# Kernel tuning notes

Hardware: AMD Instinct MI355X
Metric: run time of the kernel (lower is better)

## Reference

```python
import jax, jax.numpy as jnp
import numpy as np

B, S, E, H = 512, 128, 256, 256   # batch, seq_len, dim_embedding, dim_model (must be equal per source)
N_GLIMPSE = 1
SAMPLE_SEED = 1


def setup_inputs() -> dict:
    key = jax.random.key(0)
    ks = jax.random.split(key, 24)
    def u(k, shape, scale):
        return jax.random.uniform(k, shape, jnp.float32, -scale, scale)
    s = 1.0 / np.sqrt(H)
    return {
        "problems": jax.random.normal(ks[0], (B, S, 4), jnp.float32),
        # GraphEmbedding: linear 4 -> E
        "embed_W": u(ks[1], (4, E), 0.5),
        "embed_b": u(ks[2], (E,), 0.5),
        # encoder LSTM (PyTorch gate order i,f,g,o; b = b_ih + b_hh)
        "Wi_enc": u(ks[3], (4 * H, E), s),
        "Wh_enc": u(ks[4], (4 * H, H), s),
        "b_enc": u(ks[5], (4 * H,), s),
        # decoder LSTM
        "Wi_dec": u(ks[6], (4 * H, E), s),
        "Wh_dec": u(ks[7], (4 * H, H), s),
        "b_dec": u(ks[8], (4 * H,), s),
        # learned first decoder input
        "dec0": u(ks[9], (H,), s),
        # glimpse Bahdanau attention
        "Wq_g": u(ks[10], (H, H), s), "bq_g": u(ks[11], (H,), s),
        "Wr_g": u(ks[12], (H, H), s), "br_g": u(ks[13], (H,), s),
        "V_g": u(ks[14], (H,), s),
        # pointer Bahdanau attention
        "Wq_p": u(ks[15], (H, H), s), "bq_p": u(ks[16], (H,), s),
        "Wr_p": u(ks[17], (H, H), s), "br_p": u(ks[18], (H,), s),
        "V_p": u(ks[19], (H,), s),
    }


def _lstm_cell(x, h, c, Wi, Wh, b):
    g = x @ Wi.T + h @ Wh.T + b
    i, f, gg, o = jnp.split(g, 4, axis=-1)
    c = jax.nn.sigmoid(f) * c + jax.nn.sigmoid(i) * jnp.tanh(gg)
    h = jax.nn.sigmoid(o) * jnp.tanh(c)
    return h, c


def reference(problems, embed_W, embed_b, Wi_enc, Wh_enc, b_enc, Wi_dec, Wh_dec, b_dec,
              dec0, Wq_g, bq_g, Wr_g, br_g, V_g, Wq_p, bq_p, Wr_p, br_p, V_p):
    nb, sl = problems.shape[0], problems.shape[1]
    embd = problems @ embed_W + embed_b  # [B,S,E]

    h0 = jnp.zeros((nb, H), jnp.float32)
    def enc_step(carry, x):
        h, c = carry
        h, c = _lstm_cell(x, h, c, Wi_enc, Wh_enc, b_enc)
        return (h, c), h
    (h, c), hs = jax.lax.scan(enc_step, (h0, h0), embd.transpose(1, 0, 2))
    enc = hs.transpose(1, 0, 2)  # [B,S,H] encoder states

    # L_ref is a 1x1 conv == per-position linear; it only depends on enc, hoist out of loop
    refp_g = enc @ Wr_g.T + br_g  # [B,S,H]
    refp_p = enc @ Wr_p.T + br_p

    def attn(q, refp, Wq, bq, V):
        qp = q @ Wq.T + bq  # [B,H]
        # U[b,s] = sum_d V[d] * tanh(qp[b,d] + refp[b,s,d]) * 10
        return jnp.einsum('bsd,d->bs', jnp.tanh(qp[:, None, :] + refp) * 10.0, V)

    key = jax.random.key(SAMPLE_SEED)
    bidx = jnp.arange(nb)

    def dec_step(carry, _):
        h, c, last, visited, t = carry
        x = jnp.where(t == 0, dec0[None, :], embd[bidx, last])  # [B,E]
        h, c = _lstm_cell(x, h, c, Wi_dec, Wh_dec, b_dec)
        q = h
        for _g in range(N_GLIMPSE):
            u = attn(q, refp_g, Wq_g, bq_g, V_g)
            u = jnp.where(visited, -1e8, u)  # mask already-chosen actions
            q = jnp.einsum('bsd,bs->bd', refp_g, jax.nn.softmax(u, axis=1))
        logits = attn(q, refp_p, Wq_p, bq_p, V_p)
        logits = jnp.where(visited, -jnp.inf, logits)
        act = jax.random.categorical(jax.random.fold_in(key, t), logits)  # 'sampling'
        probs = jax.nn.softmax(logits, axis=1)
        p_sel = jnp.take_along_axis(probs, act[:, None], axis=1)[:, 0]
        visited = visited.at[bidx, act].set(True)
        return (h, c, act, visited, t + 1), (p_sel, act)

    carry0 = (h, c, jnp.zeros((nb,), jnp.int32), jnp.zeros((nb, sl), bool), jnp.int32(0))
    _, (probs_seq, acts) = jax.lax.scan(dec_step, carry0, None, length=sl)
    return probs_seq, acts  # [S,B] float probs of chosen actions, [S,B] int actions
```

## Files before the change

### kernel.cpp

```cpp
#include <hip/hip_runtime.h>
#include <math.h>
#include <stdint.h>

#define NB 512
#define SL 128

#define O_WHEF    0
#define O_WHDF    262144
#define O_WRT     524288
#define O_WQGT    655360
#define O_WQPT    720896
#define O_ME64    786432
#define O_MD64    794624
#define O_VE64    802816
#define O_VD64    804864
#define O_X064    806912
#define O_HDH     808960
#define O_HDC     1071104
#define O_RG      1333248
#define O_RP      18110464
#define O_HALL    34887680
#define O_GUM     51664896
#define WS_FLOATS 68442112

__device__ __align__(16) float g_ws[WS_FLOATS];

__device__ __forceinline__ float sigf(float x) { return 1.0f / (1.0f + expf(-x)); }

__device__ __forceinline__ float tanh_fast(float x) {
    float e = __expf(2.0f * x);
    return 1.0f - 2.0f / (e + 1.0f);
}

__device__ __forceinline__ void tf2x32(uint32_t k0, uint32_t k1, uint32_t x0, uint32_t x1,
                                       uint32_t& o0, uint32_t& o1) {
    uint32_t ks2 = k0 ^ k1 ^ 0x1BD11BDAu;
    x0 += k0; x1 += k1;
#define RR(r) { x0 += x1; x1 = (x1 << r) | (x1 >> (32 - r)); x1 ^= x0; }
    RR(13) RR(15) RR(26) RR(6)   x0 += k1;  x1 += ks2 + 1u;
    RR(17) RR(29) RR(16) RR(24)  x0 += ks2; x1 += k0 + 2u;
    RR(13) RR(15) RR(26) RR(6)   x0 += k0;  x1 += k1 + 3u;
    RR(17) RR(29) RR(16) RR(24)  x0 += k1;  x1 += ks2 + 4u;
    RR(13) RR(15) RR(26) RR(6)   x0 += ks2; x1 += k0 + 5u;
#undef RR
    o0 = x0; o1 = x1;
}

__device__ __forceinline__ double gumbel_jax(uint32_t k0, uint32_t k1, uint32_t n) {
    uint32_t o0, o1; tf2x32(k0, k1, 0u, n, o0, o1);
    uint32_t bits = o0 ^ o1;
    float f = __uint_as_float((bits >> 9) | 0x3f800000u) - 1.0f;
    f = fmaxf(f, 1.17549435e-38f);
    return -log(-log((double)f));
}

__global__ void pre_k(const float* __restrict__ embed_W, const float* __restrict__ embed_b,
                      const float* __restrict__ Wi_enc, const float* __restrict__ Wh_enc,
                      const float* __restrict__ b_enc,
                      const float* __restrict__ Wi_dec, const float* __restrict__ Wh_dec,
                      const float* __restrict__ b_dec, const float* __restrict__ dec0,
                      const float* __restrict__ Wr_g, const float* __restrict__ Wr_p,
                      const float* __restrict__ Wq_g, const float* __restrict__ Wq_p) {
    float* ws = g_ws;
    double* ME = (double*)(ws + O_ME64);
    double* MD = (double*)(ws + O_MD64);
    double* VE = (double*)(ws + O_VE64);
    double* VD = (double*)(ws + O_VD64);
    double* X0 = (double*)(ws + O_X064);
    double* GUM = (double*)(ws + O_GUM);
    int i0 = blockIdx.x * blockDim.x + threadIdx.x;
    int np = gridDim.x * blockDim.x;
    for (int i = i0; i < 262144; i += np) {
        int k = i >> 10, r = i & 1023;
        int dst = ((k >> 2) << 12) + (r << 2) + (k & 3);
        ws[O_WHEF + dst] = Wh_enc[r * 256 + k];
        ws[O_WHDF + dst] = Wh_dec[r * 256 + k];
    }
    for (int i = i0; i < 131072; i += np) {
        int k = i >> 9, col = i & 511;
        ws[O_WRT + i] = (col < 256) ? Wr_g[col * 256 + k] : Wr_p[(col - 256) * 256 + k];
    }
    for (int i = i0; i < 65536; i += np) {
        int j = i & 255, k = i >> 8;
        int dst = ((k >> 2) << 10) + (j << 2) + (k & 3);
        ws[O_WQGT + dst] = Wq_g[j * 256 + k];
        ws[O_WQPT + dst] = Wq_p[j * 256 + k];
    }
    for (int i = i0; i < 4096; i += np) {
        int e = i >> 10, r = i & 1023;
        const float* we = embed_W + e * 256;
        const float* wa = Wi_enc + r * 256;
        const float* wb = Wi_dec + r * 256;
        double a = 0.0, b = 0.0;
        for (int E = 0; E < 256; ++E) { a += (double)we[E] * wa[E]; b += (double)we[E] * wb[E]; }
        ME[i] = a; MD[i] = b;
    }
    for (int r = i0; r < 1024; r += np) {
        const float* wa = Wi_enc + r * 256;
        const float* wb = Wi_dec + r * 256;
        double a = 0.0, b = 0.0, x = 0.0;
        for (int E = 0; E < 256; ++E) {
            a += (double)embed_b[E] * wa[E];
            b += (double)embed_b[E] * wb[E];
            x += (double)dec0[E] * wb[E];
        }
        VE[r] = a + (double)b_enc[r];
        VD[r] = b + (double)b_dec[r];
        X0[r] = x + (double)b_dec[r];
    }
    for (int i = i0; i < 8388608; i += np) {
        int t = i >> 16;
        uint32_t n = (uint32_t)(i & 65535);
        uint32_t kk0, kk1;
        tf2x32(0u, 1u, 0u, (uint32_t)t, kk0, kk1);
        GUM[i] = gumbel_jax(kk0, kk1, n);
    }
}

__global__ __launch_bounds__(1024) void enc_k(const float* __restrict__ problems) {
    float* ws = g_ws;
    const float4* Wh4 = (const float4*)(ws + O_WHEF);
    const double* ME = (const double*)(ws + O_ME64);
    const double* VE = (const double*)(ws + O_VE64);
    double* HDH = (double*)(ws + O_HDH);
    double* HDC = (double*)(ws + O_HDC);
    float* Hall = ws + O_HALL;

    const int bid = blockIdx.x, tid = threadIdx.x;
    const int b0 = bid << 1;
    __shared__ __align__(16) float hf[2][256];
    __shared__ double gbuf[2][4][256];
    const float4* hf40 = (const float4*)hf[0];
    const float4* hf41 = (const float4*)hf[1];

    if (tid < 512) hf[tid >> 8][tid & 255] = 0.f;
    double c = 0.0;
    __syncthreads();

    const int g = tid >> 8, j = tid & 255;
    const double vE = VE[tid];
    const double m0 = ME[tid], m1 = ME[1024 + tid], m2 = ME[2048 + tid], m3 = ME[3072 + tid];

    for (int t = 0; t < SL; ++t) {
        float4 p0 = *(const float4*)(problems + ((size_t)b0 * SL + t) * 4);
        float4 p1 = *(const float4*)(problems + ((size_t)(b0 + 1) * SL + t) * 4);
        double a0 = vE + (double)p0.x * m0 + (double)p0.y * m1 + (double)p0.z * m2 + (double)p0.w * m3;
        double a1 = vE + (double)p1.x * m0 + (double)p1.y * m1 + (double)p1.z * m2 + (double)p1.w * m3;
        if (t > 0) {
            float f0 = 0.f, f1 = 0.f;
#pragma unroll 4
            for (int k4 = 0; k4 < 64; ++k4) {
                float4 w = Wh4[(k4 << 10) + tid];
                float4 h0 = hf40[k4], h1 = hf41[k4];
                f0 = fmaf(h0.x, w.x, f0); f1 = fmaf(h1.x, w.x, f1);
                f0 = fmaf(h0.y, w.y, f0); f1 = fmaf(h1.y, w.y, f1);
                f0 = fmaf(h0.z, w.z, f0); f1 = fmaf(h1.z, w.z, f1);
                f0 = fmaf(h0.w, w.w, f0); f1 = fmaf(h1.w, w.w, f1);
            }
            a0 += (double)f0;
            a1 += (double)f1;
        }
        gbuf[0][g][j] = a0;
        gbuf[1][g][j] = a1;
        __syncthreads();
        if (tid < 512) {
            int bb = tid >> 8, jj = tid & 255;
            double g0 = gbuf[bb][0][jj], g1 = gbuf[bb][1][jj];
            double g2 = gbuf[bb][2][jj], g3 = gbuf[bb][3][jj];
            float ig = sigf((float)g0), fg = sigf((float)g1), gt = tanhf((float)g2), og = sigf((float)g3);
            c = (double)fg * c + (double)ig * (double)gt;
            double h = (double)og * (double)tanhf((float)c);
            hf[bb][jj] = (float)h;
            Hall[((size_t)(b0 + bb) * SL + t) * 256 + jj] = (float)h;
            if (t == SL - 1) {
                HDH[(size_t)(b0 + bb) * 256 + jj] = h;
                HDC[(size_t)(b0 + bb) * 256 + jj] = c;
            }
        }
        __syncthreads();
    }
}

__global__ __launch_bounds__(256) void refp_gemm(const float* __restrict__ br_g,
                                                 const float* __restrict__ br_p) {
    float* ws = g_ws;
    const float* H = ws + O_HALL;
    const float* W = ws + O_WRT;
    const int bm = blockIdx.x, bn = blockIdx.y;
    const int tid = threadIdx.x;
    const int tr = tid >> 4, tc = tid & 15;
    __shared__ float As[32][65];
    __shared__ float Bs[32][65];
    float acc[4][4] = {};
    for (int kt = 0; kt < 8; ++kt) {
#pragma unroll
        for (int it = 0; it < 8; ++it) {
            int idx = it * 256 + tid;
            int m = idx >> 5, kk = idx & 31;
            As[kk][m] = H[(size_t)(bm * 64 + m) * 256 + kt * 32 + kk];
        }
#pragma unroll
        for (int it = 0; it < 8; ++it) {
            int idx = it * 256 + tid;
            int bk = idx >> 6, bc = idx & 63;
            Bs[bk][bc] = W[(size_t)(kt * 32 + bk) * 512 + bn * 64 + bc];
        }
        __syncthreads();
#pragma unroll
        for (int kk = 0; kk < 32; ++kk) {
            float a0 = As[kk][tr*4+0], a1 = As[kk][tr*4+1], a2 = As[kk][tr*4+2], a3 = As[kk][tr*4+3];
            float b0 = Bs[kk][tc*4+0], b1 = Bs[kk][tc*4+1], b2 = Bs[kk][tc*4+2], b3 = Bs[kk][tc*4+3];
            acc[0][0] = fmaf(a0,b0,acc[0][0]); acc[0][1] = fmaf(a0,b1,acc[0][1]);
            acc[0][2] = fmaf(a0,b2,acc[0][2]); acc[0][3] = fmaf(a0,b3,acc[0][3]);
            acc[1][0] = fmaf(a1,b0,acc[1][0]); acc[1][1] = fmaf(a1,b1,acc[1][1]);
            acc[1][2] = fmaf(a1,b2,acc[1][2]); acc[1][3] = fmaf(a1,b3,acc[1][3]);
            acc[2][0] = fmaf(a2,b0,acc[2][0]); acc[2][1] = fmaf(a2,b1,acc[2][1]);
            acc[2][2] = fmaf(a2,b2,acc[2][2]); acc[2][3] = fmaf(a2,b3,acc[2][3]);
            acc[3][0] = fmaf(a3,b0,acc[3][0]); acc[3][1] = fmaf(a3,b1,acc[3][1]);
            acc[3][2] = fmaf(a3,b2,acc[3][2]); acc[3][3] = fmaf(a3,b3,acc[3][3]);
        }
        __syncthreads();
    }
    const int colg = bn * 64 + tc * 4;
    float4 bias;
    float* outb;
    int colo;
    if (bn < 4) { bias = *(const float4*)(br_g + colg); outb = ws + O_RG; colo = colg; }
    else        { bias = *(const float4*)(br_p + colg - 256); outb = ws + O_RP; colo = colg - 256; }
#pragma unroll
    for (int i = 0; i < 4; ++i) {
        int row = bm * 64 + tr * 4 + i;
        float4 v = make_float4(acc[i][0] + bias.x, acc[i][1] + bias.y,
                               acc[i][2] + bias.z, acc[i][3] + bias.w);
        *(float4*)(outb + (size_t)row * 256 + colo) = v;
    }
}

__global__ __launch_bounds__(1024) void dec_k(const float* __restrict__ problems,
                                              const float* __restrict__ bq_g, const float* __restrict__ Vg,
                                              const float* __restrict__ bq_p, const float* __restrict__ Vp,
                                              float* __restrict__ out) {
    float* ws = g_ws;
    const float4* Wh4 = (const float4*)(ws + O_WHDF);
    const float4* WQG4 = (const float4*)(ws + O_WQGT);
    const float4* WQP4 = (const float4*)(ws + O_WQPT);
    const double* MD = (const double*)(ws + O_MD64);
    const double* VD = (const double*)(ws + O_VD64);
    const double* X0 = (const double*)(ws + O_X064);
    const double* HDH = (const double*)(ws + O_HDH);
    const double* HDC = (const double*)(ws + O_HDC);
    const double* GUM = (const double*)(ws + O_GUM);

    const int b = blockIdx.x, tid = threadIdx.x;
    __shared__ float refg_l[128][256];
    __shared__ __align__(16) float hf[256];
    __shared__ __align__(16) char scr[8192];
    double (*gbuf)[256] = (double(*)[256])scr;
    float  (*pA)[256]   = (float(*)[256])scr;
    float  (*pQ)[256]   = (float(*)[256])(scr + 4096);
    __shared__ __align__(16) float pP[4][256];
    __shared__ float u_l[128];
    __shared__ float w_l[128];
    __shared__ unsigned char vis[128];
    __shared__ int lastA;
    const float4* hf4 = (const float4*)hf;

    {
        const float4* src = (const float4*)(ws + O_RG + (size_t)b * SL * 256);
        float4* dst = (float4*)&refg_l[0][0];
        for (int i = tid; i < 8192; i += 1024) dst[i] = src[i];
    }
    double c = 0.0;
    if (tid < 256) {
        hf[tid] = (float)HDH[(size_t)b * 256 + tid];
        c = HDC[(size_t)b * 256 + tid];
    }
    if (tid < 128) vis[tid] = 0;
    if (tid == 0) lastA = 0;
    __syncthreads();

    const int g = tid >> 8, j = tid & 255;
    const int kq = tid >> 8, jj = tid & 255;
    const int wave = tid >> 6, lane = tid & 63;
    const int d0 = lane, d1 = lane + 64, d2 = lane + 128, d3 = lane + 192;
    const double vD = VD[tid], x0v = X0[tid];
    const double md0 = MD[tid], md1 = MD[1024 + tid], md2 = MD[2048 + tid], md3 = MD[3072 + tid];
    const float* refp = ws + O_RP + (size_t)b * SL * 256;
    const float* prb = problems + (size_t)b * SL * 4;

    for (int t = 0; t < SL; ++t) {
        double a0;
        if (t == 0) {
            a0 = x0v;
        } else {
            float4 p = *(const float4*)(prb + (lastA << 2));
            a0 = vD + (double)p.x * md0 + (double)p.y * md1 + (double)p.z * md2 + (double)p.w * md3;
        }
        {
            float f0 = 0.f;
#pragma unroll 4
            for (int k4 = 0; k4 < 64; ++k4) {
                float4 w = Wh4[(k4 << 10) + tid];
                float4 h = hf4[k4];
                f0 = fmaf(h.x, w.x, f0);
                f0 = fmaf(h.y, w.y, f0);
                f0 = fmaf(h.z, w.z, f0);
                f0 = fmaf(h.w, w.w, f0);
            }
            a0 += (double)f0;
        }
        gbuf[g][j] = a0;
        __syncthreads();
        if (tid < 256) {
            double g0 = gbuf[0][tid], g1 = gbuf[1][tid], g2 = gbuf[2][tid], g3 = gbuf[3][tid];
            float ig = sigf((float)g0), fg = sigf((float)g1), gt = tanhf((float)g2), og = sigf((float)g3);
            c = (double)fg * c + (double)ig * (double)gt;
            double h = (double)og * (double)tanhf((float)c);
            hf[tid] = (float)h;
        }
        __syncthreads();

        {
            const int kb4 = kq << 4;
            float qa = 0.f;
#pragma unroll 4
            for (int kk4 = 0; kk4 < 16; ++kk4) {
                float4 wq = WQG4[((kb4 + kk4) << 8) + jj];
                float4 h = hf4[kb4 + kk4];
                qa = fmaf(h.x, wq.x, qa);
                qa = fmaf(h.y, wq.y, qa);
                qa = fmaf(h.z, wq.z, qa);
                qa = fmaf(h.w, wq.w, qa);
            }
            pA[kq][jj] = qa;
        }
        __syncthreads();
        {
            const float q0 = pA[0][d0] + pA[1][d0] + pA[2][d0] + pA[3][d0] + bq_g[d0], v0 = Vg[d0];
            const float q1 = pA[0][d1] + pA[1][d1] + pA[2][d1] + pA[3][d1] + bq_g[d1], v1 = Vg[d1];
            const float q2 = pA[0][d2] + pA[1][d2] + pA[2][d2] + pA[3][d2] + bq_g[d2], v2 = Vg[d2];
            const float q3 = pA[0][d3] + pA[1][d3] + pA[2][d3] + pA[3][d3] + bq_g[d3], v3 = Vg[d3];
            const int s0 = wave << 3;
            for (int s = s0; s < s0 + 8; ++s) {
                if (vis[s]) continue;
                const float* r0 = refg_l[s];
                float part = tanh_fast(q0 + r0[d0]) * 10.f * v0;
                part = fmaf(tanh_fast(q1 + r0[d1]) * 10.f, v1, part);
                part = fmaf(tanh_fast(q2 + r0[d2]) * 10.f, v2, part);
                part = fmaf(tanh_fast(q3 + r0[d3]) * 10.f, v3, part);
                for (int off = 32; off; off >>= 1) part += __shfl_xor(part, off, 64);
                if (lane == 0) u_l[s] = part;
            }
        }
        __syncthreads();
        if (wave == 0) {
            int s1 = lane, s2 = lane + 64;
            bool v1 = vis[s1], v2 = vis[s2];
            float m = fmaxf(v1 ? -1e30f : u_l[s1], v2 ? -1e30f : u_l[s2]);
            for (int off = 32; off; off >>= 1) m = fmaxf(m, __shfl_xor(m, off, 64));
            float e1 = v1 ? 0.f : expf(u_l[s1] - m);
            float e2 = v2 ? 0.f : expf(u_l[s2] - m);
            float den = e1 + e2;
            for (int off = 32; off; off >>= 1) den += __shfl_xor(den, off, 64);
            w_l[s1] = e1 / den;
            w_l[s2] = e2 / den;
        }
        __syncthreads();
        {
            const int s0 = kq << 5;
            float q = 0.f;
            for (int s = s0; s < s0 + 32; ++s) {
                float w = w_l[s];
                if (w != 0.f) q = fmaf(w, refg_l[s][jj], q);
            }
            pQ[kq][jj] = q;
        }
        __syncthreads();
        {
            const int kb4 = kq << 4;
            float qa = 0.f;
            const float4* pQ0 = (const float4*)pQ[0];
            const float4* pQ1 = (const float4*)pQ[1];
            const float4* pQ2 = (const float4*)pQ[2];
            const float4* pQ3 = (const float4*)pQ[3];
#pragma unroll 4
            for (int kk4 = 0; kk4 < 16; ++kk4) {
                int k4 = kb4 + kk4;
                float4 wq = WQP4[(k4 << 8) + jj];
                float4 q0v = pQ0[k4], q1v = pQ1[k4], q2v = pQ2[k4], q3v = pQ3[k4];
                float qkx = ((q0v.x + q1v.x) + q2v.x) + q3v.x;
                float qky = ((q0v.y + q1v.y) + q2v.y) + q3v.y;
                float qkz = ((q0v.z + q1v.z) + q2v.z) + q3v.z;
                float qkw = ((q0v.w + q1v.w) + q2v.w) + q3v.w;
                qa = fmaf(qkx, wq.x, qa);
                qa = fmaf(qky, wq.y, qa);
                qa = fmaf(qkz, wq.z, qa);
                qa = fmaf(qkw, wq.w, qa);
            }
            pP[kq][jj] = qa;
        }
        __syncthreads();
        {
            const float q0 = pP[0][d0] + pP[1][d0] + pP[2][d0] + pP[3][d0] + bq_p[d0], v0 = Vp[d0];
            const float q1 = pP[0][d1] + pP[1][d1] + pP[2][d1] + pP[3][d1] + bq_p[d1], v1 = Vp[d1];
            const float q2 = pP[0][d2] + pP[1][d2] + pP[2][d2] + pP[3][d2] + bq_p[d2], v2 = Vp[d2];
            const float q3 = pP[0][d3] + pP[1][d3] + pP[2][d3] + pP[3][d3] + bq_p[d3], v3 = Vp[d3];
            const int s0 = wave << 3;
            for (int s = s0; s < s0 + 8; ++s) {
                if (vis[s]) continue;
                const float* r0 = refp + (s << 8);
                float part = tanh_fast(q0 + r0[d0]) * 10.f * v0;
                part = fmaf(tanh_fast(q1 + r0[d1]) * 10.f, v1, part);
                part = fmaf(tanh_fast(q2 + r0[d2]) * 10.f, v2, part);
                part = fmaf(tanh_fast(q3 + r0[d3]) * 10.f, v3, part);
                for (int off = 32; off; off >>= 1) part += __shfl_xor(part, off, 64);
                if (lane == 0) u_l[s] = part;
            }
        }
        __syncthreads();
        if (wave == 0) {
            int s1 = lane, s2 = lane + 64;
            bool v1 = vis[s1], v2 = vis[s2];
            float m = fmaxf(v1 ? -1e30f : u_l[s1], v2 ? -1e30f : u_l[s2]);
            for (int off = 32; off; off >>= 1) m = fmaxf(m, __shfl_xor(m, off, 64));
            float e1 = v1 ? 0.f : expf(u_l[s1] - m);
            float e2 = v2 ? 0.f : expf(u_l[s2] - m);
            float den = e1 + e2;
            for (int off = 32; off; off >>= 1) den += __shfl_xor(den, off, 64);
            const double* gt = GUM + ((size_t)t << 16) + (b << 7);
            double z1 = v1 ? -1.0e300 : (double)u_l[s1] + gt[s1];
            double z2 = v2 ? -1.0e300 : (double)u_l[s2] + gt[s2];
            double bz; int bi;
            if (z2 > z1) { bz = z2; bi = s2; } else { bz = z1; bi = s1; }
            for (int off = 32; off; off >>= 1) {
                double oz = __shfl_xor(bz, off, 64);
                int oi = __shfl_xor(bi, off, 64);
                if (oz > bz || (oz == bz && oi < bi)) { bz = oz; bi = oi; }
            }
            if (lane == 0) {
                float pr = expf(u_l[bi] - m) / den;
                out[t * NB + b] = pr;
                out[SL * NB + t * NB + b] = (float)bi;
                vis[bi] = 1;
                lastA = bi;
            }
        }
        __syncthreads();
    }
}

extern "C" void kernel_launch(void* const* d_in, const int* in_sizes, int n_in,
                              void* d_out, int out_size, void* d_ws, size_t ws_size,
                              hipStream_t stream) {
    (void)d_ws; (void)ws_size; (void)n_in; (void)in_sizes; (void)out_size;
    const float* problems = (const float*)d_in[0];
    const float* embed_W  = (const float*)d_in[1];
    const float* embed_b  = (const float*)d_in[2];
    const float* Wi_enc   = (const float*)d_in[3];
    const float* Wh_enc   = (const float*)d_in[4];
    const float* b_enc    = (const float*)d_in[5];
    const float* Wi_dec   = (const float*)d_in[6];
    const float* Wh_dec   = (const float*)d_in[7];
    const float* b_dec    = (const float*)d_in[8];
    const float* dec0     = (const float*)d_in[9];
    const float* Wq_g     = (const float*)d_in[10];
    const float* bq_g     = (const float*)d_in[11];
    const float* Wr_g     = (const float*)d_in[12];
    const float* br_g     = (const float*)d_in[13];
    const float* V_g      = (const float*)d_in[14];
    const float* Wq_p     = (const float*)d_in[15];
    const float* bq_p     = (const float*)d_in[16];
    const float* Wr_p     = (const float*)d_in[17];
    const float* br_p     = (const float*)d_in[18];
    const float* V_p      = (const float*)d_in[19];
    float* outp = (float*)d_out;

    hipLaunchKernelGGL(pre_k, dim3(512), dim3(256), 0, stream,
                       embed_W, embed_b, Wi_enc, Wh_enc, b_enc,
                       Wi_dec, Wh_dec, b_dec, dec0, Wr_g, Wr_p, Wq_g, Wq_p);
    hipLaunchKernelGGL(enc_k, dim3(256), dim3(1024), 0, stream, problems);
    hipLaunchKernelGGL(refp_gemm, dim3(1024, 8), dim3(256), 0, stream, br_g, br_p);
    hipLaunchKernelGGL(dec_k, dim3(512), dim3(1024), 0, stream,
                       problems, bq_g, V_g, bq_p, V_p, outp);
}
```

Measured before the change: 9.000 ms.

## Overlap next-step LSTM recurrent matvec with attention via split thread groups

```diff
diff --git a/kernel.cpp b/kernel.cpp
--- a/kernel.cpp
+++ b/kernel.cpp
@@ -254,11 +254,12 @@
     const int b = blockIdx.x, tid = threadIdx.x;
     __shared__ float refg_l[128][256];
     __shared__ __align__(16) float hf[256];
+    __shared__ float gpre[1024];
     __shared__ __align__(16) char scr[8192];
     double (*gbuf)[256] = (double(*)[256])scr;
     float  (*pA)[256]   = (float(*)[256])scr;
-    float  (*pQ)[256]   = (float(*)[256])(scr + 4096);
-    __shared__ __align__(16) float pP[4][256];
+    float  (*pQ)[256]   = (float(*)[256])(scr + 2048);
+    float  (*pP)[256]   = (float(*)[256])(scr + 4096);
     __shared__ float u_l[128];
     __shared__ float w_l[128];
     __shared__ unsigned char vis[128];
@@ -279,14 +280,47 @@
     if (tid == 0) lastA = 0;
     __syncthreads();
 
+    {
+        float f0 = 0.f;
+#pragma unroll 4
+        for (int k4 = 0; k4 < 64; ++k4) {
+            float4 w = Wh4[(k4 << 10) + tid];
+            float4 h = hf4[k4];
+            f0 = fmaf(h.x, w.x, f0);
+            f0 = fmaf(h.y, w.y, f0);
+            f0 = fmaf(h.z, w.z, f0);
+            f0 = fmaf(h.w, w.w, f0);
+        }
+        gpre[tid] = f0;
+    }
+    __syncthreads();
+
+    const bool isG = tid < 512;
+    const int stid = tid & 511;
+    const int kh = stid >> 8, jj = stid & 255;
+    const int swave = stid >> 6, lane = tid & 63;
+    const int d0 = lane, d1 = lane + 64, d2 = lane + 128, d3 = lane + 192;
     const int g = tid >> 8, j = tid & 255;
-    const int kq = tid >> 8, jj = tid & 255;
-    const int wave = tid >> 6, lane = tid & 63;
-    const int d0 = lane, d1 = lane + 64, d2 = lane + 128, d3 = lane + 192;
+    const int r0 = stid, r1 = stid + 512;
     const double vD = VD[tid], x0v = X0[tid];
     const double md0 = MD[tid], md1 = MD[1024 + tid], md2 = MD[2048 + tid], md3 = MD[3072 + tid];
     const float* refp = ws + O_RP + (size_t)b * SL * 256;
     const float* prb = problems + (size_t)b * SL * 4;
+
+    const int CB[7] = {0, 11, 22, 33, 44, 54, 64};
+
+#define G_CHUNK(ci)                                                        \
+    if (isG) {                                                             \
+        for (int k4 = CB[ci]; k4 < CB[ci + 1]; ++k4) {                     \
+            float4 wA = Wh4[(k4 << 10) + r0];                              \
+            float4 wB = Wh4[(k4 << 10) + r1];                              \
+            float4 h = hf4[k4];                                            \
+            fA = fmaf(h.x, wA.x, fA); fB = fmaf(h.x, wB.x, fB);            \
+            fA = fmaf(h.y, wA.y, fA); fB = fmaf(h.y, wB.y, fB);            \
+            fA = fmaf(h.z, wA.z, fA); fB = fmaf(h.z, wB.z, fB);            \
+            fA = fmaf(h.w, wA.w, fA); fB = fmaf(h.w, wB.w, fB);            \
+        }                                                                  \
+    }
 
     for (int t = 0; t < SL; ++t) {
         double a0;
@@ -296,19 +330,7 @@
             float4 p = *(const float4*)(prb + (lastA << 2));
             a0 = vD + (double)p.x * md0 + (double)p.y * md1 + (double)p.z * md2 + (double)p.w * md3;
         }
-        {
-            float f0 = 0.f;
-#pragma unroll 4
-            for (int k4 = 0; k4 < 64; ++k4) {
-                float4 w = Wh4[(k4 << 10) + tid];
-                float4 h = hf4[k4];
-                f0 = fmaf(h.x, w.x, f0);
-                f0 = fmaf(h.y, w.y, f0);
-                f0 = fmaf(h.z, w.z, f0);
-                f0 = fmaf(h.w, w.w, f0);
-            }
-            a0 += (double)f0;
-        }
+        a0 += (double)gpre[tid];
         gbuf[g][j] = a0;
         __syncthreads();
         if (tid < 256) {
@@ -320,40 +342,47 @@
         }
         __syncthreads();
 
-        {
-            const int kb4 = kq << 4;
+        float fA = 0.f, fB = 0.f;
+
+        G_CHUNK(0)
+        else {
             float qa = 0.f;
+            const int kb4 = kh << 5;
 #pragma unroll 4
-            for (int kk4 = 0; kk4 < 16; ++kk4) {
-                float4 wq = WQG4[((kb4 + kk4) << 8) + jj];
-                float4 h = hf4[kb4 + kk4];
+            for (int kk4 = 0; kk4 < 32; ++kk4) {
+                int k4 = kb4 + kk4;
+                float4 wq = WQG4[(k4 << 8) + jj];
+                float4 h = hf4[k4];
                 qa = fmaf(h.x, wq.x, qa);
                 qa = fmaf(h.y, wq.y, qa);
                 qa = fmaf(h.z, wq.z, qa);
                 qa = fmaf(h.w, wq.w, qa);
             }
-            pA[kq][jj] = qa;
-        }
-        __syncthreads();
-        {
-            const float q0 = pA[0][d0] + pA[1][d0] + pA[2][d0] + pA[3][d0] + bq_g[d0], v0 = Vg[d0];
-            const float q1 = pA[0][d1] + pA[1][d1] + pA[2][d1] + pA[3][d1] + bq_g[d1], v1 = Vg[d1];
-            const float q2 = pA[0][d2] + pA[1][d2] + pA[2][d2] + pA[3][d2] + bq_g[d2], v2 = Vg[d2];
-            const float q3 = pA[0][d3] + pA[1][d3] + pA[2][d3] + pA[3][d3] + bq_g[d3], v3 = Vg[d3];
-            const int s0 = wave << 3;
-            for (int s = s0; s < s0 + 8; ++s) {
+            pA[kh][jj] = qa;
+        }
+        __syncthreads();
+
+        G_CHUNK(1)
+        else {
+            const float q0 = pA[0][d0] + pA[1][d0] + bq_g[d0], v0 = Vg[d0];
+            const float q1 = pA[0][d1] + pA[1][d1] + bq_g[d1], v1 = Vg[d1];
+            const float q2 = pA[0][d2] + pA[1][d2] + bq_g[d2], v2 = Vg[d2];
+            const float q3 = pA[0][d3] + pA[1][d3] + bq_g[d3], v3 = Vg[d3];
+            for (int s = swave; s < SL; s += 8) {
                 if (vis[s]) continue;
-                const float* r0 = refg_l[s];
-                float part = tanh_fast(q0 + r0[d0]) * 10.f * v0;
-                part = fmaf(tanh_fast(q1 + r0[d1]) * 10.f, v1, part);
-                part = fmaf(tanh_fast(q2 + r0[d2]) * 10.f, v2, part);
-                part = fmaf(tanh_fast(q3 + r0[d3]) * 10.f, v3, part);
+                const float* r = refg_l[s];
+                float part = tanh_fast(q0 + r[d0]) * 10.f * v0;
+                part = fmaf(tanh_fast(q1 + r[d1]) * 10.f, v1, part);
+                part = fmaf(tanh_fast(q2 + r[d2]) * 10.f, v2, part);
+                part = fmaf(tanh_fast(q3 + r[d3]) * 10.f, v3, part);
                 for (int off = 32; off; off >>= 1) part += __shfl_xor(part, off, 64);
                 if (lane == 0) u_l[s] = part;
             }
         }
         __syncthreads();
-        if (wave == 0) {
+
+        G_CHUNK(2)
+        else if (swave == 0) {
             int s1 = lane, s2 = lane + 64;
             bool v1 = vis[s1], v2 = vis[s2];
             float m = fmaxf(v1 ? -1e30f : u_l[s1], v2 ? -1e30f : u_l[s2]);
@@ -366,59 +395,60 @@
             w_l[s2] = e2 / den;
         }
         __syncthreads();
-        {
-            const int s0 = kq << 5;
+
+        G_CHUNK(3)
+        else {
+            const int s0q = kh << 6;
             float q = 0.f;
-            for (int s = s0; s < s0 + 32; ++s) {
+            for (int s = s0q; s < s0q + 64; ++s) {
                 float w = w_l[s];
                 if (w != 0.f) q = fmaf(w, refg_l[s][jj], q);
             }
-            pQ[kq][jj] = q;
-        }
-        __syncthreads();
-        {
-            const int kb4 = kq << 4;
+            pQ[kh][jj] = q;
+        }
+        __syncthreads();
+
+        G_CHUNK(4)
+        else {
             float qa = 0.f;
+            const int kb4 = kh << 5;
             const float4* pQ0 = (const float4*)pQ[0];
             const float4* pQ1 = (const float4*)pQ[1];
-            const float4* pQ2 = (const float4*)pQ[2];
-            const float4* pQ3 = (const float4*)pQ[3];
 #pragma unroll 4
-            for (int kk4 = 0; kk4 < 16; ++kk4) {
+            for (int kk4 = 0; kk4 < 32; ++kk4) {
                 int k4 = kb4 + kk4;
                 float4 wq = WQP4[(k4 << 8) + jj];
-                float4 q0v = pQ0[k4], q1v = pQ1[k4], q2v = pQ2[k4], q3v = pQ3[k4];
-                float qkx = ((q0v.x + q1v.x) + q2v.x) + q3v.x;
-                float qky = ((q0v.y + q1v.y) + q2v.y) + q3v.y;
-                float qkz = ((q0v.z + q1v.z) + q2v.z) + q3v.z;
-                float qkw = ((q0v.w + q1v.w) + q2v.w) + q3v.w;
-                qa = fmaf(qkx, wq.x, qa);
-                qa = fmaf(qky, wq.y, qa);
-                qa = fmaf(qkz, wq.z, qa);
-                qa = fmaf(qkw, wq.w, qa);
-            }
-            pP[kq][jj] = qa;
-        }
-        __syncthreads();
-        {
-            const float q0 = pP[0][d0] + pP[1][d0] + pP[2][d0] + pP[3][d0] + bq_p[d0], v0 = Vp[d0];
-            const float q1 = pP[0][d1] + pP[1][d1] + pP[2][d1] + pP[3][d1] + bq_p[d1], v1 = Vp[d1];
-            const float q2 = pP[0][d2] + pP[1][d2] + pP[2][d2] + pP[3][d2] + bq_p[d2], v2 = Vp[d2];
-            const float q3 = pP[0][d3] + pP[1][d3] + pP[2][d3] + pP[3][d3] + bq_p[d3], v3 = Vp[d3];
-            const int s0 = wave << 3;
-            for (int s = s0; s < s0 + 8; ++s) {
+                float4 q0v = pQ0[k4], q1v = pQ1[k4];
+                qa = fmaf(q0v.x + q1v.x, wq.x, qa);
+                qa = fmaf(q0v.y + q1v.y, wq.y, qa);
+                qa = fmaf(q0v.z + q1v.z, wq.z, qa);
+                qa = fmaf(q0v.w + q1v.w, wq.w, qa);
+            }
+            pP[kh][jj] = qa;
+        }
+        __syncthreads();
+
+        G_CHUNK(5)
+        else {
+            const float q0 = pP[0][d0] + pP[1][d0] + bq_p[d0], v0 = Vp[d0];
+            const float q1 = pP[0][d1] + pP[1][d1] + bq_p[d1], v1 = Vp[d1];
+            const float q2 = pP[0][d2] + pP[1][d2] + bq_p[d2], v2 = Vp[d2];
+            const float q3 = pP[0][d3] + pP[1][d3] + bq_p[d3], v3 = Vp[d3];
+            for (int s = swave; s < SL; s += 8) {
                 if (vis[s]) continue;
-                const float* r0 = refp + (s << 8);
-                float part = tanh_fast(q0 + r0[d0]) * 10.f * v0;
-                part = fmaf(tanh_fast(q1 + r0[d1]) * 10.f, v1, part);
-                part = fmaf(tanh_fast(q2 + r0[d2]) * 10.f, v2, part);
-                part = fmaf(tanh_fast(q3 + r0[d3]) * 10.f, v3, part);
+                const float* r = refp + (s << 8);
+                float part = tanh_fast(q0 + r[d0]) * 10.f * v0;
+                part = fmaf(tanh_fast(q1 + r[d1]) * 10.f, v1, part);
+                part = fmaf(tanh_fast(q2 + r[d2]) * 10.f, v2, part);
+                part = fmaf(tanh_fast(q3 + r[d3]) * 10.f, v3, part);
                 for (int off = 32; off; off >>= 1) part += __shfl_xor(part, off, 64);
                 if (lane == 0) u_l[s] = part;
             }
         }
-        __syncthreads();
-        if (wave == 0) {
+        if (isG) { gpre[r0] = fA; gpre[r1] = fB; }
+        __syncthreads();
+
+        if (!isG && swave == 0) {
             int s1 = lane, s2 = lane + 64;
             bool v1 = vis[s1], v2 = vis[s2];
             float m = fmaxf(v1 ? -1e30f : u_l[s1], v2 ? -1e30f : u_l[s2]);
@@ -447,6 +477,7 @@
         }
         __syncthreads();
     }
+#undef G_CHUNK
 }
 
 extern "C" void kernel_launch(void* const* d_in, const int* in_sizes, int n_in,
```

Result: slower. 19.36 ms (+115.1%).
